# Kernel tuning notes

Measured on AMD Instinct MI355X. Metric: run time of the kernel, lower is better.

The kernel has to match this reference:

```python
import jax, jax.numpy as jnp
import numpy as np

N = 20000      # total nodes (100 graphs x 200 nodes)
B = 100        # batch_size
PER = 200      # nodes per graph (uniform) -> max_num_nodes
E = 320000     # edges (before self-loops)
F_IN = 32      # num_features
HEADS = 10
OUT = 128      # output_dim
NEG_SLOPE = 0.2  # PyG GATConv default


def setup_inputs() -> dict:
    key = jax.random.key(0)
    ks = jax.random.split(key, 14)
    feats = jax.random.normal(ks[0], (N, F_IN), jnp.float32)
    src = jax.random.randint(ks[1], (E,), 0, N)
    dst = jax.random.randint(ks[2], (E,), 0, N)
    edge_index = jnp.stack([src, dst]).astype(jnp.int32)
    graph_id = jnp.repeat(jnp.arange(B, dtype=jnp.int32), PER)
    batch_num_nodes = jnp.full((B,), PER, jnp.int32)
    s1 = 1.0 / np.sqrt(F_IN)
    s2 = 1.0 / np.sqrt(F_IN * HEADS)
    s3 = 1.0 / np.sqrt(OUT)
    return {
        "feats": feats,
        "edge_index": edge_index,
        "graph_id": graph_id,
        "batch_num_nodes": batch_num_nodes,
        # GATConv 1: in F_IN -> HEADS x F_IN, concat
        "W1": jax.random.normal(ks[3], (F_IN, HEADS * F_IN), jnp.float32) * s1,
        "a1_src": jax.random.normal(ks[4], (HEADS, F_IN), jnp.float32) * s1,
        "a1_dst": jax.random.normal(ks[5], (HEADS, F_IN), jnp.float32) * s1,
        "b1": jnp.zeros((HEADS * F_IN,), jnp.float32),
        "W2": jax.random.normal(ks[6], (HEADS * F_IN, OUT), jnp.float32) * s2,
        "a2_src": jax.random.normal(ks[7], (1, OUT), jnp.float32) * s3,
        "a2_dst": jax.random.normal(ks[8], (1, OUT), jnp.float32) * s3,
        "b2": jnp.zeros((OUT,), jnp.float32),
        # shared fc_g1
        "fc_w": jax.random.normal(ks[9], (OUT, OUT), jnp.float32) * s3,
        "fc_b": jnp.zeros((OUT,), jnp.float32),
    }


def gat_conv(x, src, dst, W, a_src, a_dst, bias, heads, out_dim):
    # x: [N, Fin]; src/dst already include self-loops (PyG default add_self_loops=True)
    n = x.shape[0]
    xw = (x @ W).reshape(n, heads, out_dim)                 # [N,H,F]
    s_src = jnp.einsum('nhf,hf->nh', xw, a_src)             # [N,H]
    s_dst = jnp.einsum('nhf,hf->nh', xw, a_dst)
    e = jax.nn.leaky_relu(s_src[src] + s_dst[dst], NEG_SLOPE)  # [E,H]
    # segment softmax over incoming edges of each destination node
    m = jax.ops.segment_max(e, dst, num_segments=n)         # [N,H]
    ex = jnp.exp(e - m[dst])
    denom = jax.ops.segment_sum(ex, dst, num_segments=n)    # [N,H]
    alpha = ex / jnp.maximum(denom[dst], 1e-16)             # [E,H]
    out = jax.ops.segment_sum(alpha[:, :, None] * xw[src], dst, num_segments=n)  # [N,H,F]
    return out.reshape(n, heads * out_dim) + bias


def reference(feats, edge_index, graph_id, batch_num_nodes,
              W1, a1_src, a1_dst, b1, W2, a2_src, a2_dst, b2, fc_w, fc_b):
    n = feats.shape[0]
    loops = jnp.arange(n, dtype=edge_index.dtype)
    src = jnp.concatenate([edge_index[0], loops])
    dst = jnp.concatenate([edge_index[1], loops])
    x = feats.astype(jnp.float32)
    # dropout layers are identity in eval mode
    x = jax.nn.elu(gat_conv(x, src, dst, W1, a1_src, a1_dst, b1, HEADS, F_IN))
    x = gat_conv(x, src, dst, W2, a2_src, a2_dst, b2, 1, OUT)
    x = jax.nn.relu(x)                                       # [N, OUT]
    # dgl_split: scatter node feats into [B, max_num_nodes, OUT] padded tensor
    cum = jnp.concatenate([jnp.zeros((1,), jnp.int32),
                           jnp.cumsum(batch_num_nodes).astype(jnp.int32)])
    idx = jnp.arange(n, dtype=jnp.int32) - cum[graph_id] + graph_id * PER
    padded = jnp.zeros((B * PER, OUT), x.dtype).at[idx].set(x).reshape(B, PER, OUT)
    out = jax.nn.relu(padded @ fc_w + fc_b)                  # [B, PER, OUT]
    # global max pool per graph, then shared fc_g1 + relu
    pooled = jax.ops.segment_max(x, graph_id, num_segments=B)  # [B, OUT]
    pooled = jax.nn.relu(pooled @ fc_w + fc_b)
    return (out, pooled)
```

## Files before the change

kernel.cpp:

```cpp
#include <hip/hip_runtime.h>

#define N_NODES 20000
#define N_EDGES 320000
#define ETOT    (N_EDGES + N_NODES)
#define HEADS   10
#define F_IN    32
#define C1      (HEADS * F_IN)
#define C2      128
#define NB      100
#define PER     200
#define CAP     96
#define HSTRIDE 328
#define X2STRIDE 136

typedef __attribute__((ext_vector_type(8))) short bf16x8;
typedef __attribute__((ext_vector_type(4))) float floatx4;
typedef _Float16 f16;
typedef _Float16 f16x2 __attribute__((ext_vector_type(2)));
typedef _Float16 f16x8 __attribute__((ext_vector_type(8)));

static __device__ __forceinline__ unsigned short f2bf(float f) {
    unsigned int u = __float_as_uint(f);
    unsigned int r = (u + 0x7fffu + ((u >> 16) & 1u)) >> 16;
    return (unsigned short)r;
}

#define SCAT_BLOCKS  ((ETOT + 255) / 256)
#define SCORE_BLOCKS ((N_NODES + 63) / 64)
#define W2P_BLOCKS   ((C1 * C2 + 255) / 256)
#define W1P_BLOCKS   ((HEADS * F_IN * F_IN + 255) / 256)
#define FCP_BLOCKS   ((C2 * C2 + 255) / 256)
#define F16_BLOCKS   ((N_NODES * F_IN / 4 + 255) / 256)
__global__ __launch_bounds__(256) void mega_prep_kernel(
        const int* __restrict__ ei, int* __restrict__ cursor, int* __restrict__ csr_src,
        const float* __restrict__ feats, f16* __restrict__ feats16,
        const float* __restrict__ W1, unsigned short* __restrict__ W1p,
        const float* __restrict__ W2, unsigned short* __restrict__ W2p,
        const float* __restrict__ fcw, f16* __restrict__ FCp,
        const float* __restrict__ a1s, const float* __restrict__ a1d,
        float* __restrict__ s_src, float* __restrict__ s_dst) {
    unsigned int b = blockIdx.x;
    if (b < SCAT_BLOCKS) {
        int e = b * 256 + threadIdx.x;
        if (e >= ETOT) return;
        int s, d;
        if (e < N_EDGES) { s = ei[e]; d = ei[N_EDGES + e]; }
        else             { s = e - N_EDGES; d = s; }
        int pos = atomicAdd(&cursor[d], 1);
        csr_src[(size_t)d * CAP + pos] = s;
        return;
    }
    b -= SCAT_BLOCKS;
    if (b < SCORE_BLOCKS) {
        __shared__ __align__(16) float A[64 * F_IN];
        __shared__ float Ws[C1], Wd[C1];
        int t = threadIdx.x;
        for (int o = t; o < C1; o += 256) {
            int k = o & 31, h = o >> 5;
            float ss = 0.f, dd = 0.f;
#pragma unroll
            for (int f = 0; f < F_IN; f++) {
                float wv = W1[k * C1 + h * 32 + f];
                ss += wv * a1s[h * 32 + f];
                dd += wv * a1d[h * 32 + f];
            }
            Ws[k * HEADS + h] = ss;
            Wd[k * HEADS + h] = dd;
        }
        int n0 = b * 64;
        int nrows = min(64, N_NODES - n0);
        const float4* fs = (const float4*)(feats + (size_t)n0 * F_IN);
        float4* Af = (float4*)A;
        for (int i = t; i < nrows * 8; i += 256) Af[i] = fs[i];
        __syncthreads();
        for (int o = t; o < nrows * HEADS; o += 256) {
            int nl = o / HEADS, h = o - nl * HEADS;
            const float* ar = A + nl * F_IN;
            float ss = 0.f, dd = 0.f;
#pragma unroll
            for (int k = 0; k < F_IN; k++) {
                float av = ar[k];
                ss += av * Ws[k * HEADS + h];
                dd += av * Wd[k * HEADS + h];
            }
            s_src[(size_t)(n0 + nl) * HEADS + h] = ss;
            s_dst[(size_t)(n0 + nl) * HEADS + h] = dd;
        }
        return;
    }
    b -= SCORE_BLOCKS;
    if (b < W2P_BLOCKS) {
        int o = b * 256 + threadIdx.x;
        if (o >= C1 * C2) return;
        int j    = o & 7;
        int lane = (o >> 3) & 63;
        int ct   = (o >> 9) & 7;
        int kb   = o >> 12;
        int k = kb * 32 + (lane >> 4) * 8 + j;
        int n = ct * 16 + (lane & 15);
        W2p[o] = f2bf(W2[k * C2 + n]);
        return;
    }
    b -= W2P_BLOCKS;
    if (b < W1P_BLOCKS) {
        int o = b * 256 + threadIdx.x;
        if (o >= HEADS * F_IN * F_IN) return;
        int j    = o & 7;
        int lane = (o >> 3) & 63;
        int ct   = (o >> 9) & 1;
        int h    = o >> 10;
        int k = (lane >> 4) * 8 + j;
        int f = ct * 16 + (lane & 15);
        W1p[o] = f2bf(W1[k * C1 + h * 32 + f]);
        return;
    }
    b -= W1P_BLOCKS;
    if (b < FCP_BLOCKS) {
        int o = b * 256 + threadIdx.x;
        if (o >= C2 * C2) return;
        int j    = o & 7;
        int lane = (o >> 3) & 63;
        int ct   = (o >> 9) & 7;
        int kb   = o >> 12;
        int k = kb * 32 + (lane >> 4) * 8 + j;
        int n = ct * 16 + (lane & 15);
        FCp[o] = (f16)fcw[k * C2 + n];
        return;
    }
    b -= FCP_BLOCKS;
    {
        int o = b * 256 + threadIdx.x;
        if (o < N_NODES * F_IN / 4) {
            float4 v = ((const float4*)feats)[o];
            f16* d = feats16 + 4 * o;
            d[0] = (f16)v.x; d[1] = (f16)v.y; d[2] = (f16)v.z; d[3] = (f16)v.w;
        }
    }
}

__global__ __launch_bounds__(256) void agg1h1g2_kernel(
        const f16* __restrict__ feats16, const float* __restrict__ s_src,
        const float* __restrict__ s_dst, const int* __restrict__ deg_arr,
        const int* __restrict__ csr_src,
        const unsigned short* __restrict__ W1p, const float* __restrict__ b1,
        const unsigned short* __restrict__ W2p,
        const float* __restrict__ a_src, const float* __restrict__ a_dst,
        f16* __restrict__ xw2h, float* __restrict__ s_src2, float* __restrict__ s_dst2) {
    union Smem {
        struct { f16 P[4][HEADS * 64]; int S[4][64]; } p1;
        unsigned short H[16 * HSTRIDE];
    };
    __shared__ __align__(16) Smem u;
    __shared__ __align__(16) unsigned short G[16 * HSTRIDE];
    __shared__ float redS[4][16], redD[4][16];

    int wslot = threadIdx.x >> 6;
    int lane  = threadIdx.x & 63;
    int k = lane & 31, half = lane >> 5;
    int row0 = blockIdx.x * 16;
    f16* P = u.p1.P[wslot];
    int* S = u.p1.S[wslot];
    const f16x2 ones = {(f16)1.f, (f16)1.f};
    const char* fb = (const char*)feats16 + 2 * k;

    for (int rep = 0; rep < 4; rep++) {
        int r = wslot * 4 + rep;
        int n = row0 + r;
        int beg = n * CAP, deg = deg_arr[n];
        const float* sdp = s_dst + (size_t)n * HEADS;
        float sd[10];
#pragma unroll
        for (int q = 0; q < 5; q++) {
            float2 v = *(const float2*)(sdp + 2 * q);
            sd[2 * q] = v.x; sd[2 * q + 1] = v.y;
        }
        float g[10], la[10];
#pragma unroll
        for (int h = 0; h < 10; h++) { g[h] = 0.f; la[h] = 0.f; }

        for (int c0 = 0; c0 < deg; c0 += 64) {
            int dc = min(deg - c0, 64);
            bool act = lane < dc;
            int s_e = csr_src[beg + c0 + min(lane, dc - 1)];
            const float* ssp = s_src + (size_t)s_e * HEADS;
            float p[10];
#pragma unroll
            for (int q = 0; q < 5; q++) {
                float2 v = *(const float2*)(ssp + 2 * q);
                float e0 = v.x + sd[2 * q];
                float e1 = v.y + sd[2 * q + 1];
                e0 = (e0 >= 0.f) ? e0 : 0.2f * e0;
                e1 = (e1 >= 0.f) ? e1 : 0.2f * e1;
                p[2 * q]     = act ? __expf(e0) : 0.f;
                p[2 * q + 1] = act ? __expf(e1) : 0.f;
            }
            S[lane] = s_e << 6;
#pragma unroll
            for (int h = 0; h < 10; h++) P[h * 64 + lane] = (f16)p[h];
            asm volatile("s_waitcnt lgkmcnt(0)" ::: "memory");

            int dcp = (dc + 3) & ~3;
            for (int i = 0; i < dcp; i += 4) {
                int e0 = i + half * 2;
                int2 ss2 = *(const int2*)&S[e0];
                f16x2 v;
                v.x = *(const f16*)(fb + ss2.x);
                v.y = *(const f16*)(fb + ss2.y);
#pragma unroll
                for (int h = 0; h < 10; h++) {
                    f16x2 pp = *(const f16x2*)&P[h * 64 + e0];
                    g[h]  = __builtin_amdgcn_fdot2(pp, v, g[h], false);
                    la[h] = __builtin_amdgcn_fdot2(pp, ones, la[h], false);
                }
            }
            asm volatile("s_waitcnt lgkmcnt(0)" ::: "memory");
        }
#pragma unroll
        for (int h = 0; h < 10; h++) {
            g[h]  += __shfl_xor(g[h], 32);
            la[h] += __shfl_xor(la[h], 32);
        }
        if (half == 0) {
#pragma unroll
            for (int h = 0; h < 10; h++)
                G[r * HSTRIDE + h * 32 + k] = f2bf(g[h] / fmaxf(la[h], 1e-16f));
        }
    }
    __syncthreads();

    int quad = lane >> 4, col = lane & 15;
    for (int h = wslot; h < 10; h += 4) {
        bf16x8 a = *(const bf16x8*)&G[col * HSTRIDE + h * 32 + quad * 8];
        bf16x8 bA = ((const bf16x8*)W1p)[(h * 2 + 0) * 64 + lane];
        bf16x8 bB = ((const bf16x8*)W1p)[(h * 2 + 1) * 64 + lane];
        floatx4 z = {0.f, 0.f, 0.f, 0.f};
        floatx4 c0 = __builtin_amdgcn_mfma_f32_16x16x32_bf16(a, bA, z, 0, 0, 0);
        floatx4 c1 = __builtin_amdgcn_mfma_f32_16x16x32_bf16(a, bB, z, 0, 0, 0);
        float bias0 = b1[h * 32 + col];
        float bias1 = b1[h * 32 + 16 + col];
#pragma unroll
        for (int reg = 0; reg < 4; reg++) {
            int rr = quad * 4 + reg;
            float o0 = c0[reg] + bias0;
            float o1 = c1[reg] + bias1;
            o0 = (o0 > 0.f) ? o0 : (__expf(o0) - 1.f);
            o1 = (o1 > 0.f) ? o1 : (__expf(o1) - 1.f);
            u.H[rr * HSTRIDE + h * 32 + col]      = f2bf(o0);
            u.H[rr * HSTRIDE + h * 32 + 16 + col] = f2bf(o1);
        }
    }
    __syncthreads();

    floatx4 acc[2];
    acc[0] = (floatx4){0.f, 0.f, 0.f, 0.f};
    acc[1] = (floatx4){0.f, 0.f, 0.f, 0.f};
    const bf16x8* pb = (const bf16x8*)W2p;
#pragma unroll
    for (int kb = 0; kb < 10; kb++) {
        bf16x8 a = *(const bf16x8*)&u.H[col * HSTRIDE + kb * 32 + quad * 8];
#pragma unroll
        for (int c = 0; c < 2; c++) {
            bf16x8 b = pb[(kb * 8 + (2 * wslot + c)) * 64 + lane];
            acc[c] = __builtin_amdgcn_mfma_f32_16x16x32_bf16(a, b, acc[c], 0, 0, 0);
        }
    }
    float asv[2], adv[2];
#pragma unroll
    for (int c = 0; c < 2; c++) {
        asv[c] = a_src[(2 * wslot + c) * 16 + col];
        adv[c] = a_dst[(2 * wslot + c) * 16 + col];
    }
#pragma unroll
    for (int reg = 0; reg < 4; reg++) {
        int row = row0 + quad * 4 + reg;
        float vs = 0.f, vd = 0.f;
#pragma unroll
        for (int c = 0; c < 2; c++) {
            float v = acc[c][reg];
            xw2h[(size_t)row * C2 + (2 * wslot + c) * 16 + col] = (f16)v;
            vs += v * asv[c];
            vd += v * adv[c];
        }
#pragma unroll
        for (int off = 8; off >= 1; off >>= 1) {
            vs += __shfl_xor(vs, off);
            vd += __shfl_xor(vd, off);
        }
        if (col == 0) { redS[wslot][quad * 4 + reg] = vs; redD[wslot][quad * 4 + reg] = vd; }
    }
    __syncthreads();
    if (wslot == 0) {
        if (lane < 16)
            s_src2[row0 + lane] = redS[0][lane] + redS[1][lane] + redS[2][lane] + redS[3][lane];
        else if (lane < 32) {
            int r2 = lane - 16;
            s_dst2[row0 + r2] = redD[0][r2] + redD[1][r2] + redD[2][r2] + redD[3][r2];
        }
    }
}

__global__ __launch_bounds__(256) void agg2fc_kernel(
        const f16* __restrict__ xw2h, const float* __restrict__ s_src2,
        const float* __restrict__ s_dst2, const int* __restrict__ deg_arr,
        const int* __restrict__ csr_src, const float* __restrict__ b2,
        const f16* __restrict__ FCp, const float* __restrict__ fcb,
        float* __restrict__ out, int* __restrict__ pooledi) {
    __shared__ __align__(8) int2 shE[4][64];
    __shared__ __align__(16) f16 X[16 * X2STRIDE];
    int wslot = threadIdx.x >> 6;
    int lane = threadIdx.x & 63;
    int row0 = blockIdx.x * 16;
    int2* E = shE[wslot];
    const char* xb = (const char*)xw2h + 4 * lane;

#pragma unroll
    for (int rep = 0; rep < 4; rep++) {
        int r = wslot * 4 + rep;
        int n = row0 + r;
        int beg = n * CAP, deg = deg_arr[n];
        float sd = s_dst2[n];
        float l = 0.f, a0 = 0.f, a1 = 0.f;

        for (int c0 = 0; c0 < deg; c0 += 64) {
            int dc = min(deg - c0, 64);
            bool act = lane < dc;
            int s_e = csr_src[beg + c0 + min(lane, dc - 1)];
            float e = s_src2[s_e] + sd;
            e = (e >= 0.f) ? e : 0.2f * e;
            float p = act ? __expf(e) : 0.f;
            float su = p;
#pragma unroll
            for (int off = 32; off >= 1; off >>= 1) su += __shfl_xor(su, off);
            l += su;

            E[lane] = make_int2(s_e << 8, __float_as_int(p));
            asm volatile("s_waitcnt lgkmcnt(0)" ::: "memory");

            int dcr = (dc + 3) & ~3;
            for (int i = 0; i < dcr; i += 4) {
                int2 e0 = E[i + 0], e1 = E[i + 1], e2 = E[i + 2], e3 = E[i + 3];
                f16x2 v0 = *(const f16x2*)(xb + e0.x);
                f16x2 v1 = *(const f16x2*)(xb + e1.x);
                f16x2 v2 = *(const f16x2*)(xb + e2.x);
                f16x2 v3 = *(const f16x2*)(xb + e3.x);
                float p0 = __int_as_float(e0.y), p1 = __int_as_float(e1.y);
                float p2 = __int_as_float(e2.y), p3 = __int_as_float(e3.y);
                a0 += p0 * (float)v0.x + p1 * (float)v1.x + p2 * (float)v2.x + p3 * (float)v3.x;
                a1 += p0 * (float)v0.y + p1 * (float)v1.y + p2 * (float)v2.y + p3 * (float)v3.y;
            }
            asm volatile("s_waitcnt lgkmcnt(0)" ::: "memory");
        }

        float linv = 1.f / fmaxf(l, 1e-16f);
        float2 bb = *(const float2*)(b2 + 2 * lane);
        f16x2 o;
        o.x = (f16)fmaxf(a0 * linv + bb.x, 0.f);
        o.y = (f16)fmaxf(a1 * linv + bb.y, 0.f);
        *(f16x2*)&X[r * X2STRIDE + 2 * lane] = o;
    }
    __syncthreads();

    int quad = lane >> 4, col = lane & 15;
    floatx4 acc[2];
    acc[0] = (floatx4){0.f, 0.f, 0.f, 0.f};
    acc[1] = (floatx4){0.f, 0.f, 0.f, 0.f};
    const f16x8* pb = (const f16x8*)FCp;
#pragma unroll
    for (int kb = 0; kb < 4; kb++) {
        f16x8 a = *(const f16x8*)&X[(lane & 15) * X2STRIDE + kb * 32 + quad * 8];
#pragma unroll
        for (int c = 0; c < 2; c++) {
            int ct = wslot * 2 + c;
            f16x8 b = pb[(kb * 8 + ct) * 64 + lane];
            acc[c] = __builtin_amdgcn_mfma_f32_16x16x32_f16(a, b, acc[c], 0, 0, 0);
        }
    }
#pragma unroll
    for (int c = 0; c < 2; c++) {
        int ct = wslot * 2 + c;
        float bias = fcb[ct * 16 + col];
#pragma unroll
        for (int reg = 0; reg < 4; reg++) {
            int row = row0 + quad * 4 + reg;
            out[(size_t)row * C2 + ct * 16 + col] = fmaxf(acc[c][reg] + bias, 0.f);
        }
    }

    if (threadIdx.x < C2) {
        int c = threadIdx.x;
        int gA = row0 / PER;
        int gB = (row0 + 15) / PER;
        float mA = 0.f, mB = 0.f;
#pragma unroll
        for (int r = 0; r < 16; r++) {
            float v = (float)X[r * X2STRIDE + c];
            if ((row0 + r) / PER == gA) mA = fmaxf(mA, v);
            else                        mB = fmaxf(mB, v);
        }
        atomicMax(&pooledi[gA * C2 + c], __float_as_int(mA));
        if (gB != gA) atomicMax(&pooledi[gB * C2 + c], __float_as_int(mB));
    }
}

__global__ void poolfc_kernel(const int* __restrict__ pooledi, const float* __restrict__ fcw,
                              const float* __restrict__ fcb, float* __restrict__ outp) {
    __shared__ float mx[C2];
    int g = blockIdx.x, t = threadIdx.x;
    mx[t] = __int_as_float(pooledi[g * C2 + t]);
    __syncthreads();
    float acc = 0.f;
    for (int k = 0; k < C2; k++) acc += mx[k] * fcw[k * C2 + t];
    outp[g * C2 + t] = fmaxf(acc + fcb[t], 0.f);
}

extern "C" void kernel_launch(void* const* d_in, const int* in_sizes, int n_in,
                              void* d_out, int out_size, void* d_ws, size_t ws_size,
                              hipStream_t stream) {
    const float* feats = (const float*)d_in[0];
    const int*   ei    = (const int*)d_in[1];
    const float* W1  = (const float*)d_in[4];
    const float* a1s = (const float*)d_in[5];
    const float* a1d = (const float*)d_in[6];
    const float* b1  = (const float*)d_in[7];
    const float* W2  = (const float*)d_in[8];
    const float* a2s = (const float*)d_in[9];
    const float* a2d = (const float*)d_in[10];
    const float* b2  = (const float*)d_in[11];
    const float* fcw = (const float*)d_in[12];
    const float* fcb = (const float*)d_in[13];

    float* out_main = (float*)d_out;
    float* out_pool = (float*)d_out + (size_t)N_NODES * C2;

    char* p = (char*)d_ws;
    auto alloc = [&](size_t bytes) {
        char* r = p;
        p += (bytes + 255) & ~(size_t)255;
        return r;
    };
    unsigned short* W2p  = (unsigned short*)alloc(sizeof(short) * C1 * C2);
    unsigned short* W1p  = (unsigned short*)alloc(sizeof(short) * HEADS * F_IN * F_IN);
    f16*   FCp     = (f16*)alloc(sizeof(f16) * C2 * C2);
    f16*   feats16 = (f16*)alloc(sizeof(f16) * (size_t)N_NODES * F_IN);
    f16*   xw2h    = (f16*)alloc(sizeof(f16) * (size_t)N_NODES * C2);
    float* s1s    = (float*)alloc(sizeof(float) * N_NODES * HEADS);
    float* s1d    = (float*)alloc(sizeof(float) * N_NODES * HEADS);
    float* s2s    = (float*)alloc(sizeof(float) * N_NODES);
    float* s2d    = (float*)alloc(sizeof(float) * N_NODES);
    const int NZ = N_NODES + NB * C2;
    int* zeros   = (int*)alloc(sizeof(int) * NZ);
    int* cursor  = zeros;
    int* pooledi = zeros + N_NODES;
    int* csr_src = (int*)alloc(sizeof(int) * N_NODES * CAP);

    hipMemsetAsync(zeros, 0, sizeof(int) * NZ, stream);

    mega_prep_kernel<<<SCAT_BLOCKS + SCORE_BLOCKS + W2P_BLOCKS + W1P_BLOCKS + FCP_BLOCKS + F16_BLOCKS,
                       256, 0, stream>>>(
        ei, cursor, csr_src, feats, feats16, W1, W1p, W2, W2p, fcw, FCp,
        a1s, a1d, s1s, s1d);

    agg1h1g2_kernel<<<1250, 256, 0, stream>>>(feats16, s1s, s1d, cursor, csr_src,
                                              W1p, b1, W2p, a2s, a2d, xw2h, s2s, s2d);
    agg2fc_kernel<<<1250, 256, 0, stream>>>(xw2h, s2s, s2d, cursor, csr_src, b2,
                                            FCp, fcb, out_main, pooledi);
    poolfc_kernel<<<NB, C2, 0, stream>>>(pooledi, fcw, fcb, out_pool);
}
```

Before: 162.8 us.

## Split agg1 edges per half-wave, partition agg2 gathers by source, fuse pool-FC

```diff
diff --git a/kernel.cpp b/kernel.cpp
--- a/kernel.cpp
+++ b/kernel.cpp
@@ -12,6 +12,7 @@
 #define CAP     96
 #define HSTRIDE 328
 #define X2STRIDE 136
+#define SPLIT   10000
 
 typedef __attribute__((ext_vector_type(8))) short bf16x8;
 typedef __attribute__((ext_vector_type(4))) float floatx4;
@@ -147,7 +148,7 @@
         const float* __restrict__ a_src, const float* __restrict__ a_dst,
         f16* __restrict__ xw2h, float* __restrict__ s_src2, float* __restrict__ s_dst2) {
     union Smem {
-        struct { f16 P[4][HEADS * 64]; int S[4][64]; } p1;
+        struct { f16 P[4][2][HEADS * 32]; int S[4][2][32]; } p1;
         unsigned short H[16 * HSTRIDE];
     };
     __shared__ __align__(16) Smem u;
@@ -156,15 +157,15 @@
 
     int wslot = threadIdx.x >> 6;
     int lane  = threadIdx.x & 63;
-    int k = lane & 31, half = lane >> 5;
+    int l = lane & 31, half = lane >> 5;
     int row0 = blockIdx.x * 16;
-    f16* P = u.p1.P[wslot];
-    int* S = u.p1.S[wslot];
+    f16* P = u.p1.P[wslot][half];
+    int* S = u.p1.S[wslot][half];
     const f16x2 ones = {(f16)1.f, (f16)1.f};
-    const char* fb = (const char*)feats16 + 2 * k;
-
-    for (int rep = 0; rep < 4; rep++) {
-        int r = wslot * 4 + rep;
+    const char* fb = (const char*)feats16 + 2 * l;
+
+    for (int rep = 0; rep < 2; rep++) {
+        int r = wslot * 4 + rep * 2 + half;
         int n = row0 + r;
         int beg = n * CAP, deg = deg_arr[n];
         const float* sdp = s_dst + (size_t)n * HEADS;
@@ -178,10 +179,10 @@
 #pragma unroll
         for (int h = 0; h < 10; h++) { g[h] = 0.f; la[h] = 0.f; }
 
-        for (int c0 = 0; c0 < deg; c0 += 64) {
-            int dc = min(deg - c0, 64);
-            bool act = lane < dc;
-            int s_e = csr_src[beg + c0 + min(lane, dc - 1)];
+        for (int c0 = 0; c0 < deg; c0 += 32) {
+            int dc = min(deg - c0, 32);
+            bool act = l < dc;
+            int s_e = csr_src[beg + c0 + min(l, dc - 1)];
             const float* ssp = s_src + (size_t)s_e * HEADS;
             float p[10];
 #pragma unroll
@@ -194,37 +195,30 @@
                 p[2 * q]     = act ? __expf(e0) : 0.f;
                 p[2 * q + 1] = act ? __expf(e1) : 0.f;
             }
-            S[lane] = s_e << 6;
-#pragma unroll
-            for (int h = 0; h < 10; h++) P[h * 64 + lane] = (f16)p[h];
+            S[l] = s_e << 6;
+#pragma unroll
+            for (int h = 0; h < 10; h++) P[h * 32 + l] = (f16)p[h];
             asm volatile("s_waitcnt lgkmcnt(0)" ::: "memory");
 
-            int dcp = (dc + 3) & ~3;
-            for (int i = 0; i < dcp; i += 4) {
-                int e0 = i + half * 2;
-                int2 ss2 = *(const int2*)&S[e0];
+            int dcp = (dc + 1) & ~1;
+            for (int i = 0; i < dcp; i += 2) {
+                int2 ss2 = *(const int2*)&S[i];
                 f16x2 v;
                 v.x = *(const f16*)(fb + ss2.x);
                 v.y = *(const f16*)(fb + ss2.y);
 #pragma unroll
                 for (int h = 0; h < 10; h++) {
-                    f16x2 pp = *(const f16x2*)&P[h * 64 + e0];
+                    f16x2 pp = *(const f16x2*)&P[h * 32 + i];
                     g[h]  = __builtin_amdgcn_fdot2(pp, v, g[h], false);
                     la[h] = __builtin_amdgcn_fdot2(pp, ones, la[h], false);
                 }
             }
             asm volatile("s_waitcnt lgkmcnt(0)" ::: "memory");
         }
-#pragma unroll
-        for (int h = 0; h < 10; h++) {
-            g[h]  += __shfl_xor(g[h], 32);
-            la[h] += __shfl_xor(la[h], 32);
-        }
-        if (half == 0) {
-#pragma unroll
-            for (int h = 0; h < 10; h++)
-                G[r * HSTRIDE + h * 32 + k] = f2bf(g[h] / fmaxf(la[h], 1e-16f));
-        }
+        unsigned short* gr = &G[r * HSTRIDE + l];
+#pragma unroll
+        for (int h = 0; h < 10; h++)
+            gr[h * 32] = f2bf(g[h] / fmaxf(la[h], 1e-16f));
     }
     __syncthreads();
 
@@ -304,9 +298,14 @@
         const float* __restrict__ s_dst2, const int* __restrict__ deg_arr,
         const int* __restrict__ csr_src, const float* __restrict__ b2,
         const f16* __restrict__ FCp, const float* __restrict__ fcb,
-        float* __restrict__ out, int* __restrict__ pooledi) {
+        const float* __restrict__ fcw,
+        float* __restrict__ out, float* __restrict__ outp,
+        int* __restrict__ pooledi, int* __restrict__ done) {
     __shared__ __align__(8) int2 shE[4][64];
     __shared__ __align__(16) f16 X[16 * X2STRIDE];
+    __shared__ float pool_mx[C2];
+    __shared__ float pool_part[2 * C2];
+    __shared__ int win_s[2];
     int wslot = threadIdx.x >> 6;
     int lane = threadIdx.x & 63;
     int row0 = blockIdx.x * 16;
@@ -333,22 +332,30 @@
             for (int off = 32; off >= 1; off >>= 1) su += __shfl_xor(su, off);
             l += su;
 
-            E[lane] = make_int2(s_e << 8, __float_as_int(p));
-            asm volatile("s_waitcnt lgkmcnt(0)" ::: "memory");
-
-            int dcr = (dc + 3) & ~3;
-            for (int i = 0; i < dcr; i += 4) {
-                int2 e0 = E[i + 0], e1 = E[i + 1], e2 = E[i + 2], e3 = E[i + 3];
-                f16x2 v0 = *(const f16x2*)(xb + e0.x);
-                f16x2 v1 = *(const f16x2*)(xb + e1.x);
-                f16x2 v2 = *(const f16x2*)(xb + e2.x);
-                f16x2 v3 = *(const f16x2*)(xb + e3.x);
-                float p0 = __int_as_float(e0.y), p1 = __int_as_float(e1.y);
-                float p2 = __int_as_float(e2.y), p3 = __int_as_float(e3.y);
-                a0 += p0 * (float)v0.x + p1 * (float)v1.x + p2 * (float)v2.x + p3 * (float)v3.x;
-                a1 += p0 * (float)v0.y + p1 * (float)v1.y + p2 * (float)v2.y + p3 * (float)v3.y;
+#pragma unroll
+            for (int sw = 0; sw < 2; sw++) {
+                bool sel = act && (sw ? (s_e >= SPLIT) : (s_e < SPLIT));
+                unsigned long long m = __ballot(sel);
+                int cnt = __popcll(m);
+                int pos = __popcll(m & ((1ull << lane) - 1ull));
+                if (sel) E[pos] = make_int2(s_e << 8, __float_as_int(p));
+                int cntp = (cnt + 3) & ~3;
+                if (lane >= cnt && lane < cntp) E[lane] = make_int2(0, 0);
+                asm volatile("s_waitcnt lgkmcnt(0)" ::: "memory");
+
+                for (int i = 0; i < cntp; i += 4) {
+                    int2 e0 = E[i + 0], e1 = E[i + 1], e2 = E[i + 2], e3 = E[i + 3];
+                    f16x2 v0 = *(const f16x2*)(xb + e0.x);
+                    f16x2 v1 = *(const f16x2*)(xb + e1.x);
+                    f16x2 v2 = *(const f16x2*)(xb + e2.x);
+                    f16x2 v3 = *(const f16x2*)(xb + e3.x);
+                    float p0 = __int_as_float(e0.y), p1 = __int_as_float(e1.y);
+                    float p2 = __int_as_float(e2.y), p3 = __int_as_float(e3.y);
+                    a0 += p0 * (float)v0.x + p1 * (float)v1.x + p2 * (float)v2.x + p3 * (float)v3.x;
+                    a1 += p0 * (float)v0.y + p1 * (float)v1.y + p2 * (float)v2.y + p3 * (float)v3.y;
+                }
+                asm volatile("s_waitcnt lgkmcnt(0)" ::: "memory");
             }
-            asm volatile("s_waitcnt lgkmcnt(0)" ::: "memory");
         }
 
         float linv = 1.f / fmaxf(l, 1e-16f);
@@ -386,10 +393,10 @@
         }
     }
 
+    int gA = row0 / PER;
+    int gB = (row0 + 15) / PER;
     if (threadIdx.x < C2) {
         int c = threadIdx.x;
-        int gA = row0 / PER;
-        int gB = (row0 + 15) / PER;
         float mA = 0.f, mB = 0.f;
 #pragma unroll
         for (int r = 0; r < 16; r++) {
@@ -400,17 +407,35 @@
         atomicMax(&pooledi[gA * C2 + c], __float_as_int(mA));
         if (gB != gA) atomicMax(&pooledi[gB * C2 + c], __float_as_int(mB));
     }
-}
-
-__global__ void poolfc_kernel(const int* __restrict__ pooledi, const float* __restrict__ fcw,
-                              const float* __restrict__ fcb, float* __restrict__ outp) {
-    __shared__ float mx[C2];
-    int g = blockIdx.x, t = threadIdx.x;
-    mx[t] = __int_as_float(pooledi[g * C2 + t]);
-    __syncthreads();
-    float acc = 0.f;
-    for (int k = 0; k < C2; k++) acc += mx[k] * fcw[k * C2 + t];
-    outp[g * C2 + t] = fmaxf(acc + fcb[t], 0.f);
+    __syncthreads();
+
+    if (threadIdx.x == 0) {
+        __threadfence();
+        int tA = atomicAdd(&done[gA], 1);
+        int wA = (tA == 12);
+        int wB = 0;
+        if (gB != gA) { int tB = atomicAdd(&done[gB], 1); wB = (tB == 12); }
+        win_s[0] = wA; win_s[1] = wB;
+    }
+    __syncthreads();
+
+    auto pool_fc = [&](int g) {
+        int t = threadIdx.x;
+        if (t < C2)
+            pool_mx[t] = __int_as_float(atomicMax(&pooledi[g * C2 + t], 0));
+        __syncthreads();
+        int pc = t & (C2 - 1), piece = t >> 7;
+        float acc2 = 0.f;
+        const float* fw = fcw + (size_t)(piece * 64) * C2 + pc;
+        const float* mp = pool_mx + piece * 64;
+        for (int k = 0; k < 64; k++) acc2 += mp[k] * fw[(size_t)k * C2];
+        pool_part[piece * C2 + pc] = acc2;
+        __syncthreads();
+        if (piece == 0)
+            outp[(size_t)g * C2 + pc] = fmaxf(pool_part[pc] + pool_part[C2 + pc] + fcb[pc], 0.f);
+    };
+    if (win_s[0]) pool_fc(gA);
+    if (win_s[1]) pool_fc(gB);
 }
 
 extern "C" void kernel_launch(void* const* d_in, const int* in_sizes, int n_in,
@@ -447,10 +472,11 @@
     float* s1d    = (float*)alloc(sizeof(float) * N_NODES * HEADS);
     float* s2s    = (float*)alloc(sizeof(float) * N_NODES);
     float* s2d    = (float*)alloc(sizeof(float) * N_NODES);
-    const int NZ = N_NODES + NB * C2;
+    const int NZ = N_NODES + NB * C2 + NB;
     int* zeros   = (int*)alloc(sizeof(int) * NZ);
     int* cursor  = zeros;
     int* pooledi = zeros + N_NODES;
+    int* done    = zeros + N_NODES + NB * C2;
     int* csr_src = (int*)alloc(sizeof(int) * N_NODES * CAP);
 
     hipMemsetAsync(zeros, 0, sizeof(int) * NZ, stream);
@@ -463,6 +489,6 @@
     agg1h1g2_kernel<<<1250, 256, 0, stream>>>(feats16, s1s, s1d, cursor, csr_src,
                                               W1p, b1, W2p, a2s, a2d, xw2h, s2s, s2d);
     agg2fc_kernel<<<1250, 256, 0, stream>>>(xw2h, s2s, s2d, cursor, csr_src, b2,
-                                            FCp, fcb, out_main, pooledi);
-    poolfc_kernel<<<NB, C2, 0, stream>>>(pooledi, fcw, fcb, out_pool);
+                                            FCp, fcb, fcw, out_main, out_pool,
+                                            pooledi, done);
 }
```

New measurement: 202.5 us. 1.24x slower.

## Assign one half-wave per destination row and double block size to 512 threads

Applied to the files above, without the earlier changes.

```diff
diff --git a/kernel.cpp b/kernel.cpp
--- a/kernel.cpp
+++ b/kernel.cpp
@@ -17,6 +17,7 @@
 typedef __attribute__((ext_vector_type(4))) float floatx4;
 typedef _Float16 f16;
 typedef _Float16 f16x2 __attribute__((ext_vector_type(2)));
+typedef _Float16 f16x4 __attribute__((ext_vector_type(4)));
 typedef _Float16 f16x8 __attribute__((ext_vector_type(8)));
 
 static __device__ __forceinline__ unsigned short f2bf(float f) {
@@ -138,7 +139,7 @@
     }
 }
 
-__global__ __launch_bounds__(256) void agg1h1g2_kernel(
+__global__ __launch_bounds__(512) void agg1h1g2_kernel(
         const f16* __restrict__ feats16, const float* __restrict__ s_src,
         const float* __restrict__ s_dst, const int* __restrict__ deg_arr,
         const int* __restrict__ csr_src,
@@ -147,24 +148,25 @@
         const float* __restrict__ a_src, const float* __restrict__ a_dst,
         f16* __restrict__ xw2h, float* __restrict__ s_src2, float* __restrict__ s_dst2) {
     union Smem {
-        struct { f16 P[4][HEADS * 64]; int S[4][64]; } p1;
+        struct { f16 P[16][HEADS * 32]; int S[16][32]; } p1;
         unsigned short H[16 * HSTRIDE];
     };
     __shared__ __align__(16) Smem u;
     __shared__ __align__(16) unsigned short G[16 * HSTRIDE];
-    __shared__ float redS[4][16], redD[4][16];
-
-    int wslot = threadIdx.x >> 6;
-    int lane  = threadIdx.x & 63;
-    int k = lane & 31, half = lane >> 5;
-    int row0 = blockIdx.x * 16;
-    f16* P = u.p1.P[wslot];
-    int* S = u.p1.S[wslot];
+    __shared__ float redS[8][16], redD[8][16];
+
+    int tid   = threadIdx.x;
+    int wslot = tid >> 6;
+    int lane  = tid & 63;
+    int r     = tid >> 5;
+    int l     = tid & 31;
+    int row0  = blockIdx.x * 16;
+    f16* P = u.p1.P[r];
+    int* S = u.p1.S[r];
     const f16x2 ones = {(f16)1.f, (f16)1.f};
-    const char* fb = (const char*)feats16 + 2 * k;
-
-    for (int rep = 0; rep < 4; rep++) {
-        int r = wslot * 4 + rep;
+    const char* fb = (const char*)feats16 + 2 * l;
+
+    {
         int n = row0 + r;
         int beg = n * CAP, deg = deg_arr[n];
         const float* sdp = s_dst + (size_t)n * HEADS;
@@ -178,10 +180,10 @@
 #pragma unroll
         for (int h = 0; h < 10; h++) { g[h] = 0.f; la[h] = 0.f; }
 
-        for (int c0 = 0; c0 < deg; c0 += 64) {
-            int dc = min(deg - c0, 64);
-            bool act = lane < dc;
-            int s_e = csr_src[beg + c0 + min(lane, dc - 1)];
+        for (int c0 = 0; c0 < deg; c0 += 32) {
+            int dc = min(deg - c0, 32);
+            bool act = l < dc;
+            int s_e = csr_src[beg + c0 + min(l, dc - 1)];
             const float* ssp = s_src + (size_t)s_e * HEADS;
             float p[10];
 #pragma unroll
@@ -194,42 +196,35 @@
                 p[2 * q]     = act ? __expf(e0) : 0.f;
                 p[2 * q + 1] = act ? __expf(e1) : 0.f;
             }
-            S[lane] = s_e << 6;
-#pragma unroll
-            for (int h = 0; h < 10; h++) P[h * 64 + lane] = (f16)p[h];
+            S[l] = s_e << 6;
+#pragma unroll
+            for (int h = 0; h < 10; h++) P[h * 32 + l] = (f16)p[h];
             asm volatile("s_waitcnt lgkmcnt(0)" ::: "memory");
 
-            int dcp = (dc + 3) & ~3;
-            for (int i = 0; i < dcp; i += 4) {
-                int e0 = i + half * 2;
-                int2 ss2 = *(const int2*)&S[e0];
+            int dcp = (dc + 1) & ~1;
+            for (int i = 0; i < dcp; i += 2) {
+                int2 ss2 = *(const int2*)&S[i];
                 f16x2 v;
                 v.x = *(const f16*)(fb + ss2.x);
                 v.y = *(const f16*)(fb + ss2.y);
 #pragma unroll
                 for (int h = 0; h < 10; h++) {
-                    f16x2 pp = *(const f16x2*)&P[h * 64 + e0];
+                    f16x2 pp = *(const f16x2*)&P[h * 32 + i];
                     g[h]  = __builtin_amdgcn_fdot2(pp, v, g[h], false);
                     la[h] = __builtin_amdgcn_fdot2(pp, ones, la[h], false);
                 }
             }
             asm volatile("s_waitcnt lgkmcnt(0)" ::: "memory");
         }
-#pragma unroll
-        for (int h = 0; h < 10; h++) {
-            g[h]  += __shfl_xor(g[h], 32);
-            la[h] += __shfl_xor(la[h], 32);
-        }
-        if (half == 0) {
-#pragma unroll
-            for (int h = 0; h < 10; h++)
-                G[r * HSTRIDE + h * 32 + k] = f2bf(g[h] / fmaxf(la[h], 1e-16f));
-        }
+        unsigned short* gr = &G[r * HSTRIDE + l];
+#pragma unroll
+        for (int h = 0; h < 10; h++)
+            gr[h * 32] = f2bf(g[h] / fmaxf(la[h], 1e-16f));
     }
     __syncthreads();
 
     int quad = lane >> 4, col = lane & 15;
-    for (int h = wslot; h < 10; h += 4) {
+    for (int h = wslot; h < 10; h += 8) {
         bf16x8 a = *(const bf16x8*)&G[col * HSTRIDE + h * 32 + quad * 8];
         bf16x8 bA = ((const bf16x8*)W1p)[(h * 2 + 0) * 64 + lane];
         bf16x8 bB = ((const bf16x8*)W1p)[(h * 2 + 1) * 64 + lane];
@@ -251,36 +246,22 @@
     }
     __syncthreads();
 
-    floatx4 acc[2];
-    acc[0] = (floatx4){0.f, 0.f, 0.f, 0.f};
-    acc[1] = (floatx4){0.f, 0.f, 0.f, 0.f};
+    floatx4 acc = {0.f, 0.f, 0.f, 0.f};
     const bf16x8* pb = (const bf16x8*)W2p;
 #pragma unroll
     for (int kb = 0; kb < 10; kb++) {
         bf16x8 a = *(const bf16x8*)&u.H[col * HSTRIDE + kb * 32 + quad * 8];
-#pragma unroll
-        for (int c = 0; c < 2; c++) {
-            bf16x8 b = pb[(kb * 8 + (2 * wslot + c)) * 64 + lane];
-            acc[c] = __builtin_amdgcn_mfma_f32_16x16x32_bf16(a, b, acc[c], 0, 0, 0);
-        }
-    }
-    float asv[2], adv[2];
-#pragma unroll
-    for (int c = 0; c < 2; c++) {
-        asv[c] = a_src[(2 * wslot + c) * 16 + col];
-        adv[c] = a_dst[(2 * wslot + c) * 16 + col];
-    }
+        bf16x8 b = pb[(kb * 8 + wslot) * 64 + lane];
+        acc = __builtin_amdgcn_mfma_f32_16x16x32_bf16(a, b, acc, 0, 0, 0);
+    }
+    float asv = a_src[wslot * 16 + col];
+    float adv = a_dst[wslot * 16 + col];
 #pragma unroll
     for (int reg = 0; reg < 4; reg++) {
         int row = row0 + quad * 4 + reg;
-        float vs = 0.f, vd = 0.f;
-#pragma unroll
-        for (int c = 0; c < 2; c++) {
-            float v = acc[c][reg];
-            xw2h[(size_t)row * C2 + (2 * wslot + c) * 16 + col] = (f16)v;
-            vs += v * asv[c];
-            vd += v * adv[c];
-        }
+        float v = acc[reg];
+        xw2h[(size_t)row * C2 + wslot * 16 + col] = (f16)v;
+        float vs = v * asv, vd = v * adv;
 #pragma unroll
         for (int off = 8; off >= 1; off >>= 1) {
             vs += __shfl_xor(vs, off);
@@ -290,112 +271,113 @@
     }
     __syncthreads();
     if (wslot == 0) {
-        if (lane < 16)
-            s_src2[row0 + lane] = redS[0][lane] + redS[1][lane] + redS[2][lane] + redS[3][lane];
-        else if (lane < 32) {
+        if (lane < 16) {
+            float s = 0.f;
+#pragma unroll
+            for (int w2 = 0; w2 < 8; w2++) s += redS[w2][lane];
+            s_src2[row0 + lane] = s;
+        } else if (lane < 32) {
             int r2 = lane - 16;
-            s_dst2[row0 + r2] = redD[0][r2] + redD[1][r2] + redD[2][r2] + redD[3][r2];
-        }
-    }
-}
-
-__global__ __launch_bounds__(256) void agg2fc_kernel(
+            float d = 0.f;
+#pragma unroll
+            for (int w2 = 0; w2 < 8; w2++) d += redD[w2][r2];
+            s_dst2[row0 + r2] = d;
+        }
+    }
+}
+
+__global__ __launch_bounds__(512) void agg2fc_kernel(
         const f16* __restrict__ xw2h, const float* __restrict__ s_src2,
         const float* __restrict__ s_dst2, const int* __restrict__ deg_arr,
         const int* __restrict__ csr_src, const float* __restrict__ b2,
         const f16* __restrict__ FCp, const float* __restrict__ fcb,
         float* __restrict__ out, int* __restrict__ pooledi) {
-    __shared__ __align__(8) int2 shE[4][64];
+    __shared__ __align__(8) int2 shE[16][32];
     __shared__ __align__(16) f16 X[16 * X2STRIDE];
-    int wslot = threadIdx.x >> 6;
-    int lane = threadIdx.x & 63;
-    int row0 = blockIdx.x * 16;
-    int2* E = shE[wslot];
-    const char* xb = (const char*)xw2h + 4 * lane;
-
-#pragma unroll
-    for (int rep = 0; rep < 4; rep++) {
-        int r = wslot * 4 + rep;
+    int tid   = threadIdx.x;
+    int wslot = tid >> 6;
+    int lane  = tid & 63;
+    int r     = tid >> 5;
+    int l     = tid & 31;
+    int row0  = blockIdx.x * 16;
+    int2* E = shE[r];
+    const char* xb = (const char*)xw2h + 8 * l;
+
+    {
         int n = row0 + r;
         int beg = n * CAP, deg = deg_arr[n];
         float sd = s_dst2[n];
-        float l = 0.f, a0 = 0.f, a1 = 0.f;
-
-        for (int c0 = 0; c0 < deg; c0 += 64) {
-            int dc = min(deg - c0, 64);
-            bool act = lane < dc;
-            int s_e = csr_src[beg + c0 + min(lane, dc - 1)];
+        float ldn = 0.f, a0 = 0.f, a1 = 0.f, a2 = 0.f, a3 = 0.f;
+
+        for (int c0 = 0; c0 < deg; c0 += 32) {
+            int dc = min(deg - c0, 32);
+            bool act = l < dc;
+            int s_e = csr_src[beg + c0 + min(l, dc - 1)];
             float e = s_src2[s_e] + sd;
             e = (e >= 0.f) ? e : 0.2f * e;
             float p = act ? __expf(e) : 0.f;
             float su = p;
 #pragma unroll
-            for (int off = 32; off >= 1; off >>= 1) su += __shfl_xor(su, off);
-            l += su;
-
-            E[lane] = make_int2(s_e << 8, __float_as_int(p));
+            for (int off = 16; off >= 1; off >>= 1) su += __shfl_xor(su, off);
+            ldn += su;
+
+            E[l] = make_int2(s_e << 8, __float_as_int(p));
             asm volatile("s_waitcnt lgkmcnt(0)" ::: "memory");
 
             int dcr = (dc + 3) & ~3;
             for (int i = 0; i < dcr; i += 4) {
                 int2 e0 = E[i + 0], e1 = E[i + 1], e2 = E[i + 2], e3 = E[i + 3];
-                f16x2 v0 = *(const f16x2*)(xb + e0.x);
-                f16x2 v1 = *(const f16x2*)(xb + e1.x);
-                f16x2 v2 = *(const f16x2*)(xb + e2.x);
-                f16x2 v3 = *(const f16x2*)(xb + e3.x);
+                f16x4 v0 = *(const f16x4*)(xb + e0.x);
+                f16x4 v1 = *(const f16x4*)(xb + e1.x);
+                f16x4 v2 = *(const f16x4*)(xb + e2.x);
+                f16x4 v3 = *(const f16x4*)(xb + e3.x);
                 float p0 = __int_as_float(e0.y), p1 = __int_as_float(e1.y);
                 float p2 = __int_as_float(e2.y), p3 = __int_as_float(e3.y);
-                a0 += p0 * (float)v0.x + p1 * (float)v1.x + p2 * (float)v2.x + p3 * (float)v3.x;
-                a1 += p0 * (float)v0.y + p1 * (float)v1.y + p2 * (float)v2.y + p3 * (float)v3.y;
+                a0 += p0 * (float)v0[0] + p1 * (float)v1[0] + p2 * (float)v2[0] + p3 * (float)v3[0];
+                a1 += p0 * (float)v0[1] + p1 * (float)v1[1] + p2 * (float)v2[1] + p3 * (float)v3[1];
+                a2 += p0 * (float)v0[2] + p1 * (float)v1[2] + p2 * (float)v2[2] + p3 * (float)v3[2];
+                a3 += p0 * (float)v0[3] + p1 * (float)v1[3] + p2 * (float)v2[3] + p3 * (float)v3[3];
             }
             asm volatile("s_waitcnt lgkmcnt(0)" ::: "memory");
         }
 
-        float linv = 1.f / fmaxf(l, 1e-16f);
-        float2 bb = *(const float2*)(b2 + 2 * lane);
-        f16x2 o;
-        o.x = (f16)fmaxf(a0 * linv + bb.x, 0.f);
-        o.y = (f16)fmaxf(a1 * linv + bb.y, 0.f);
-        *(f16x2*)&X[r * X2STRIDE + 2 * lane] = o;
+        float linv = 1.f / fmaxf(ldn, 1e-16f);
+        float4 bb = *(const float4*)(b2 + 4 * l);
+        f16x4 o;
+        o[0] = (f16)fmaxf(a0 * linv + bb.x, 0.f);
+        o[1] = (f16)fmaxf(a1 * linv + bb.y, 0.f);
+        o[2] = (f16)fmaxf(a2 * linv + bb.z, 0.f);
+        o[3] = (f16)fmaxf(a3 * linv + bb.w, 0.f);
+        *(f16x4*)&X[r * X2STRIDE + 4 * l] = o;
     }
     __syncthreads();
 
     int quad = lane >> 4, col = lane & 15;
-    floatx4 acc[2];
-    acc[0] = (floatx4){0.f, 0.f, 0.f, 0.f};
-    acc[1] = (floatx4){0.f, 0.f, 0.f, 0.f};
+    floatx4 acc = {0.f, 0.f, 0.f, 0.f};
     const f16x8* pb = (const f16x8*)FCp;
 #pragma unroll
     for (int kb = 0; kb < 4; kb++) {
-        f16x8 a = *(const f16x8*)&X[(lane & 15) * X2STRIDE + kb * 32 + quad * 8];
-#pragma unroll
-        for (int c = 0; c < 2; c++) {
-            int ct = wslot * 2 + c;
-            f16x8 b = pb[(kb * 8 + ct) * 64 + lane];
-            acc[c] = __builtin_amdgcn_mfma_f32_16x16x32_f16(a, b, acc[c], 0, 0, 0);
-        }
-    }
-#pragma unroll
-    for (int c = 0; c < 2; c++) {
-        int ct = wslot * 2 + c;
-        float bias = fcb[ct * 16 + col];
-#pragma unroll
-        for (int reg = 0; reg < 4; reg++) {
-            int row = row0 + quad * 4 + reg;
-            out[(size_t)row * C2 + ct * 16 + col] = fmaxf(acc[c][reg] + bias, 0.f);
-        }
-    }
-
-    if (threadIdx.x < C2) {
-        int c = threadIdx.x;
+        f16x8 a = *(const f16x8*)&X[col * X2STRIDE + kb * 32 + quad * 8];
+        f16x8 b = pb[(kb * 8 + wslot) * 64 + lane];
+        acc = __builtin_amdgcn_mfma_f32_16x16x32_f16(a, b, acc, 0, 0, 0);
+    }
+    float bias = fcb[wslot * 16 + col];
+#pragma unroll
+    for (int reg = 0; reg < 4; reg++) {
+        int row = row0 + quad * 4 + reg;
+        out[(size_t)row * C2 + wslot * 16 + col] = fmaxf(acc[reg] + bias, 0.f);
+    }
+
+    if (tid < C2) {
+        int c = tid;
         int gA = row0 / PER;
         int gB = (row0 + 15) / PER;
         float mA = 0.f, mB = 0.f;
 #pragma unroll
-        for (int r = 0; r < 16; r++) {
-            float v = (float)X[r * X2STRIDE + c];
-            if ((row0 + r) / PER == gA) mA = fmaxf(mA, v);
-            else                        mB = fmaxf(mB, v);
+        for (int rr = 0; rr < 16; rr++) {
+            float v = (float)X[rr * X2STRIDE + c];
+            if ((row0 + rr) / PER == gA) mA = fmaxf(mA, v);
+            else                         mB = fmaxf(mB, v);
         }
         atomicMax(&pooledi[gA * C2 + c], __float_as_int(mA));
         if (gB != gA) atomicMax(&pooledi[gB * C2 + c], __float_as_int(mB));
@@ -460,9 +442,9 @@
         ei, cursor, csr_src, feats, feats16, W1, W1p, W2, W2p, fcw, FCp,
         a1s, a1d, s1s, s1d);
 
-    agg1h1g2_kernel<<<1250, 256, 0, stream>>>(feats16, s1s, s1d, cursor, csr_src,
+    agg1h1g2_kernel<<<1250, 512, 0, stream>>>(feats16, s1s, s1d, cursor, csr_src,
                                               W1p, b1, W2p, a2s, a2d, xw2h, s2s, s2d);
-    agg2fc_kernel<<<1250, 256, 0, stream>>>(xw2h, s2s, s2d, cursor, csr_src, b2,
+    agg2fc_kernel<<<1250, 512, 0, stream>>>(xw2h, s2s, s2d, cursor, csr_src, b2,
                                             FCp, fcb, out_main, pooledi);
     poolfc_kernel<<<NB, C2, 0, stream>>>(pooledi, fcw, fcb, out_pool);
 }
```

Result: faster. 157.9 us (-3.0%).
